# Performance work log

Measured on AMD Instinct MI355X. Metric: run time of the kernel, lower is better.

Reference implementation:

```python
import jax, jax.numpy as jnp
import numpy as np

N = 50000      # nodes
E = 800000     # edges (before self-loops)
F_IN = 256     # num_features
H = 8          # heads (conv1)
C = 32         # hidden_size per head (conv1)
OUT = 2        # conv2 out channels (1 head)
NEG_SLOPE = 0.2


def setup_inputs() -> dict:
    key = jax.random.key(0)
    ks = jax.random.split(key, 12)
    x = jax.random.normal(ks[0], (N, F_IN), jnp.float32)
    edge_index = jax.random.randint(ks[1], (2, E), 0, N, dtype=jnp.int64)

    def glorot(k, shape):
        fan = shape[0] if len(shape) == 2 else int(np.prod(shape))
        s = float(np.sqrt(6.0 / (fan + shape[-1])))
        return jax.random.uniform(k, shape, jnp.float32, -s, s)

    W1 = glorot(ks[2], (F_IN, H * C))
    att_src1 = glorot(ks[3], (H, C))
    att_dst1 = glorot(ks[4], (H, C))
    b1 = jnp.zeros((H * C,), jnp.float32)
    W2 = glorot(ks[5], (H * C, 1 * OUT))
    att_src2 = glorot(ks[6], (1, OUT))
    att_dst2 = glorot(ks[7], (1, OUT))
    b2 = jnp.zeros((OUT,), jnp.float32)
    return {"x": x, "edge_index": edge_index, "W1": W1, "att_src1": att_src1,
            "att_dst1": att_dst1, "b1": b1, "W2": W2, "att_src2": att_src2,
            "att_dst2": att_dst2, "b2": b2}


def gat_conv(x, src, dst, W, a_src, a_dst, b, heads, ch, n):
    # x: [n, f] -> projected [n, heads, ch]
    xp = (x @ W).reshape(n, heads, ch)
    alpha_src = jnp.einsum('nhc,hc->nh', xp, a_src)   # [n, H]
    alpha_dst = jnp.einsum('nhc,hc->nh', xp, a_dst)   # [n, H]
    e = jax.nn.leaky_relu(alpha_src[src] + alpha_dst[dst], NEG_SLOPE)  # [E', H]
    # segment softmax over edges grouped by destination node
    m = jax.ops.segment_max(e, dst, num_segments=n)                    # [n, H]
    p = jnp.exp(e - m[dst])
    denom = jax.ops.segment_sum(p, dst, num_segments=n)                # [n, H]
    alpha = p / denom[dst]                                             # [E', H]
    # weighted scatter-aggregate of source messages
    out = jax.ops.segment_sum(xp[src] * alpha[:, :, None], dst, num_segments=n)
    return out.reshape(n, heads * ch) + b


def reference(x, edge_index, W1, att_src1, att_dst1, b1, W2, att_src2, att_dst2, b2):
    n = x.shape[0]
    loops = jnp.arange(n, dtype=edge_index.dtype)  # GATConv add_self_loops=True
    src = jnp.concatenate([edge_index[0], loops])
    dst = jnp.concatenate([edge_index[1], loops])
    h = jax.nn.relu(gat_conv(x, src, dst, W1, att_src1, att_dst1, b1, H, C, n))
    # eval mode: F.dropout and attention dropout are identity
    return gat_conv(h, src, dst, W2, att_src2, att_dst2, b2, 1, OUT, n)
```

## Files before the change

kernel.cpp:

```cpp
#include <hip/hip_runtime.h>
#include <math.h>

#define N_NODES 50000
#define N_EDGES 800000
#define EP (N_EDGES + N_NODES)
#define NEG 0.2f
#define SCAN_BLOCKS 49

typedef __attribute__((ext_vector_type(8))) short bf16x8;
typedef __attribute__((ext_vector_type(4))) float f32x4;
typedef __attribute__((ext_vector_type(2))) float f32x2;

static __device__ __forceinline__ unsigned short bf16_rn(float f) {
    union { float f; unsigned int u; } v; v.f = f;
    unsigned int u = v.u;
    unsigned int r = (u + 0x7FFFu + ((u >> 16) & 1u)) >> 16;
    return (unsigned short)r;
}
static __device__ __forceinline__ float bf16_tof(unsigned short u) {
    union { unsigned int u; float f; } v; v.u = ((unsigned int)u) << 16;
    return v.f;
}
static __device__ __forceinline__ f32x2 bf2_unpack(unsigned int u) {
    union { unsigned int i; float f; } a, b;
    a.i = u << 16; b.i = u & 0xFFFF0000u;
    return (f32x2){a.f, b.f};
}


__global__ void k_hist(const int* __restrict__ ei, int* __restrict__ counts) {
    int e = blockIdx.x * 256 + threadIdx.x;
    if (e >= EP) return;
    int d = (e < N_EDGES) ? ei[N_EDGES + e] : (e - N_EDGES);
    atomicAdd(&counts[d], 1);
}

__global__ void k_scan_block(const int* __restrict__ counts, int* __restrict__ excl,
                             int* __restrict__ bsums) {
    __shared__ int wsum[4];
    int b = blockIdx.x, t = threadIdx.x;
    int lane = t & 63, w = t >> 6;
    int i0 = b * 1024 + t * 4;
    int v0 = (i0 + 0 < N_NODES) ? counts[i0 + 0] : 0;
    int v1 = (i0 + 1 < N_NODES) ? counts[i0 + 1] : 0;
    int v2 = (i0 + 2 < N_NODES) ? counts[i0 + 2] : 0;
    int v3 = (i0 + 3 < N_NODES) ? counts[i0 + 3] : 0;
    int s = v0 + v1 + v2 + v3;
    int incl = s;
    #pragma unroll
    for (int d = 1; d < 64; d <<= 1) {
        int u = __shfl_up(incl, d);
        if (lane >= d) incl += u;
    }
    if (lane == 63) wsum[w] = incl;
    __syncthreads();
    if (t == 0) {
        int run = 0;
        #pragma unroll
        for (int i = 0; i < 4; ++i) { int x = wsum[i]; wsum[i] = run; run += x; }
        bsums[b] = run;
    }
    __syncthreads();
    int base = wsum[w] + incl - s;
    if (i0 + 0 < N_NODES) excl[i0 + 0] = base;
    if (i0 + 1 < N_NODES) excl[i0 + 1] = base + v0;
    if (i0 + 2 < N_NODES) excl[i0 + 2] = base + v0 + v1;
    if (i0 + 3 < N_NODES) excl[i0 + 3] = base + v0 + v1 + v2;
}

__global__ void k_scan_add(int* __restrict__ row_ptr, const int* __restrict__ bsums) {
    __shared__ int soff;
    int b = blockIdx.x, t = threadIdx.x;
    if (t < 64) {
        int v = (t < SCAN_BLOCKS) ? bsums[t] : 0;
        int incl = v;
        #pragma unroll
        for (int d = 1; d < 64; d <<= 1) {
            int u = __shfl_up(incl, d);
            if (t >= d) incl += u;
        }
        if (t == b) soff = incl - v;
    }
    __syncthreads();
    int off = soff;
    int i0 = b * 1024 + t * 4;
    #pragma unroll
    for (int j = 0; j < 4; ++j)
        if (i0 + j < N_NODES) row_ptr[i0 + j] += off;
    if (b == 0 && t == 0) row_ptr[N_NODES] = EP;
}

__global__ void k_scatter(const int* __restrict__ ei, const int* __restrict__ row_ptr,
                          int* __restrict__ fill, int* __restrict__ colb) {
    int e = blockIdx.x * 256 + threadIdx.x;
    if (e >= EP) return;
    int s, d;
    if (e < N_EDGES) { s = ei[e]; d = ei[N_EDGES + e]; }
    else             { s = e - N_EDGES; d = s; }
    int pos = row_ptr[d] + atomicAdd(&fill[d], 1);
    colb[pos] = s;
}

__global__ void k_cvtWfrag(const float* __restrict__ W1, bf16x8* __restrict__ Wfrag) {
    int ft = blockIdx.x * 256 + threadIdx.x;
    int c = ft >> 10, rem = ft & 1023;
    int nt = rem >> 6, l = rem & 63;
    int n = (l & 15) * 16 + nt;
    int k0 = c * 32 + (l >> 4) * 8;
    bf16x8 f;
    #pragma unroll
    for (int j = 0; j < 8; ++j)
        f[j] = (short)bf16_rn(W1[(k0 + j) * 256 + n]);
    Wfrag[ft] = f;
}

#define GM_GRID 782
__global__ __launch_bounds__(128) void
k_gemm1m(const float* __restrict__ x, const bf16x8* __restrict__ Wfrag,
         unsigned short* __restrict__ xp1b,
         const float* __restrict__ asrc, const float* __restrict__ adst,
         float* __restrict__ as1, float* __restrict__ ad1) {
    __shared__ bf16x8 lds[1024];
    int t = threadIdx.x, l = t & 63, w = t >> 6;
    int rowbase = blockIdx.x * 64 + w * 32;
    int m = l & 15, kg = l >> 4;

    f32x4 acc0[16], acc1[16];
    #pragma unroll
    for (int nt = 0; nt < 16; ++nt) {
        acc0[nt] = (f32x4){0.f, 0.f, 0.f, 0.f};
        acc1[nt] = (f32x4){0.f, 0.f, 0.f, 0.f};
    }

    int r0 = rowbase + m;
    int r1 = rowbase + 16 + m;
    if (r0 > N_NODES - 1) r0 = N_NODES - 1;
    if (r1 > N_NODES - 1) r1 = N_NODES - 1;
    const float4* x4 = (const float4*)x;

    for (int c = 0; c < 8; ++c) {
        __syncthreads();
        const bf16x8* src = Wfrag + c * 1024;
        #pragma unroll
        for (int q = 0; q < 8; ++q)
            lds[q * 128 + t] = src[q * 128 + t];
        __syncthreads();

        int kb = (c * 32 + kg * 8) >> 2;
        float4 xa0 = x4[r0 * 64 + kb], xb0 = x4[r0 * 64 + kb + 1];
        float4 xa1 = x4[r1 * 64 + kb], xb1 = x4[r1 * 64 + kb + 1];
        bf16x8 aF0, aF1;
        aF0[0] = (short)bf16_rn(xa0.x); aF0[1] = (short)bf16_rn(xa0.y);
        aF0[2] = (short)bf16_rn(xa0.z); aF0[3] = (short)bf16_rn(xa0.w);
        aF0[4] = (short)bf16_rn(xb0.x); aF0[5] = (short)bf16_rn(xb0.y);
        aF0[6] = (short)bf16_rn(xb0.z); aF0[7] = (short)bf16_rn(xb0.w);
        aF1[0] = (short)bf16_rn(xa1.x); aF1[1] = (short)bf16_rn(xa1.y);
        aF1[2] = (short)bf16_rn(xa1.z); aF1[3] = (short)bf16_rn(xa1.w);
        aF1[4] = (short)bf16_rn(xb1.x); aF1[5] = (short)bf16_rn(xb1.y);
        aF1[6] = (short)bf16_rn(xb1.z); aF1[7] = (short)bf16_rn(xb1.w);

        #pragma unroll
        for (int nt = 0; nt < 16; ++nt) {
            bf16x8 bF = lds[nt * 64 + l];
            acc0[nt] = __builtin_amdgcn_mfma_f32_16x16x32_bf16(aF0, bF, acc0[nt], 0, 0, 0);
            acc1[nt] = __builtin_amdgcn_mfma_f32_16x16x32_bf16(aF1, bF, acc1[nt], 0, 0, 0);
        }
    }

    int cbase = l & 15, rq = l >> 4;
    float asV[16], adV[16];
    #pragma unroll
    for (int q = 0; q < 4; ++q) {
        float4 sa = ((const float4*)asrc)[cbase * 4 + q];
        float4 da = ((const float4*)adst)[cbase * 4 + q];
        asV[q * 4 + 0] = sa.x; asV[q * 4 + 1] = sa.y; asV[q * 4 + 2] = sa.z; asV[q * 4 + 3] = sa.w;
        adV[q * 4 + 0] = da.x; adV[q * 4 + 1] = da.y; adV[q * 4 + 2] = da.z; adV[q * 4 + 3] = da.w;
    }
    #pragma unroll
    for (int g = 0; g < 2; ++g) {
        f32x4* A = g ? acc1 : acc0;
        #pragma unroll
        for (int reg = 0; reg < 4; ++reg) {
            int gr = rowbase + g * 16 + rq * 4 + reg;
            unsigned int ob[8];
            float ps = 0.f, pd = 0.f;
            #pragma unroll
            for (int q = 0; q < 8; ++q) {
                float v0 = A[2 * q][reg], v1 = A[2 * q + 1][reg];
                ob[q] = (unsigned int)bf16_rn(v0) | ((unsigned int)bf16_rn(v1) << 16);
                ps = fmaf(v0, asV[2 * q], ps);     ps = fmaf(v1, asV[2 * q + 1], ps);
                pd = fmaf(v0, adV[2 * q], pd);     pd = fmaf(v1, adV[2 * q + 1], pd);
            }
            ps += __shfl_xor(ps, 1);
            pd += __shfl_xor(pd, 1);
            if (gr < N_NODES) {
                uint4* dst = (uint4*)(xp1b + gr * 256 + cbase * 16);
                dst[0] = make_uint4(ob[0], ob[1], ob[2], ob[3]);
                dst[1] = make_uint4(ob[4], ob[5], ob[6], ob[7]);
                if ((l & 1) == 0) {
                    as1[gr * 8 + (cbase >> 1)] = ps;
                    ad1[gr * 8 + (cbase >> 1)] = pd;
                }
            }
        }
    }
}

__global__ void k_agg1(const ushort4* __restrict__ xpb, const float* __restrict__ as1,
                       const float* __restrict__ ad1, const int* __restrict__ row_ptr,
                       const int* __restrict__ colb, const float* __restrict__ b1,
                       const float* __restrict__ W2, const float* __restrict__ as2w,
                       const float* __restrict__ ad2w,
                       float* __restrict__ xp2, float* __restrict__ as2,
                       float* __restrict__ ad2) {
    int t = threadIdx.x, l = t & 63, w = t >> 6;
    int n = blockIdx.x * 4 + w;
    int hidx = l >> 3;
    float adn = ad1[n * 8 + hidx];
    int start = row_ptr[n], end = row_ptr[n + 1];
    const uint2* xp2v = (const uint2*)xpb;
    f32x2 accA = {0.f, 0.f}, accB = {0.f, 0.f};
    float den = 0.f;
    int j = start;
    for (; j + 4 <= end; j += 4) {
        int s0 = colb[j], s1 = colb[j + 1], s2 = colb[j + 2], s3 = colb[j + 3];
        uint2 r0 = xp2v[s0 * 64 + l];
        uint2 r1 = xp2v[s1 * 64 + l];
        uint2 r2 = xp2v[s2 * 64 + l];
        uint2 r3 = xp2v[s3 * 64 + l];
        float e0 = as1[s0 * 8 + hidx] + adn;
        float e1 = as1[s1 * 8 + hidx] + adn;
        float e2 = as1[s2 * 8 + hidx] + adn;
        float e3 = as1[s3 * 8 + hidx] + adn;
        e0 = (e0 > 0.f) ? e0 : NEG * e0;
        e1 = (e1 > 0.f) ? e1 : NEG * e1;
        e2 = (e2 > 0.f) ? e2 : NEG * e2;
        e3 = (e3 > 0.f) ? e3 : NEG * e3;
        float p0 = __expf(e0), p1 = __expf(e1), p2 = __expf(e2), p3 = __expf(e3);
        den += (p0 + p1) + (p2 + p3);
        f32x2 q0 = {p0, p0}, q1 = {p1, p1}, q2 = {p2, p2}, q3 = {p3, p3};
        accA += q0 * bf2_unpack(r0.x);  accB += q0 * bf2_unpack(r0.y);
        accA += q1 * bf2_unpack(r1.x);  accB += q1 * bf2_unpack(r1.y);
        accA += q2 * bf2_unpack(r2.x);  accB += q2 * bf2_unpack(r2.y);
        accA += q3 * bf2_unpack(r3.x);  accB += q3 * bf2_unpack(r3.y);
    }
    for (; j < end; ++j) {
        int s = colb[j];
        uint2 r = xp2v[s * 64 + l];
        float e = as1[s * 8 + hidx] + adn;
        e = (e > 0.f) ? e : NEG * e;
        float p = __expf(e);
        den += p;
        f32x2 q = {p, p};
        accA += q * bf2_unpack(r.x);
        accB += q * bf2_unpack(r.y);
    }
    float4 bv = ((const float4*)b1)[l];
    float inv = 1.f / den;
    float4 o;
    o.x = fmaxf(accA[0] * inv + bv.x, 0.f);
    o.y = fmaxf(accA[1] * inv + bv.y, 0.f);
    o.z = fmaxf(accB[0] * inv + bv.z, 0.f);
    o.w = fmaxf(accB[1] * inv + bv.w, 0.f);
    float4 wa = ((const float4*)W2)[2 * l];
    float4 wb = ((const float4*)W2)[2 * l + 1];
    float d0 = o.x * wa.x + o.y * wa.z + o.z * wb.x + o.w * wb.z;
    float d1 = o.x * wa.y + o.y * wa.w + o.z * wb.y + o.w * wb.w;
    #pragma unroll
    for (int m = 1; m < 64; m <<= 1) {
        d0 += __shfl_xor(d0, m);
        d1 += __shfl_xor(d1, m);
    }
    if (l == 0) {
        xp2[2 * n] = d0;
        xp2[2 * n + 1] = d1;
        as2[n] = d0 * as2w[0] + d1 * as2w[1];
        ad2[n] = d0 * ad2w[0] + d1 * ad2w[1];
    }
}

__global__ void k_agg2(const float* __restrict__ xp2, const float* __restrict__ as2,
                       const float* __restrict__ ad2, const int* __restrict__ row_ptr,
                       const int* __restrict__ colb, const float* __restrict__ b2,
                       float* __restrict__ out) {
    int t = threadIdx.x, l = t & 63, w = t >> 6;
    int n = blockIdx.x * 4 + w;
    int start = row_ptr[n], end = row_ptr[n + 1];
    float adn = ad2[n];
    float a0 = 0.f, a1 = 0.f, den = 0.f;
    for (int j = start + l; j < end; j += 64) {
        int s = colb[j];
        float e = as2[s] + adn;
        e = (e > 0.f) ? e : NEG * e;
        float p = __expf(e);
        den += p;
        a0 = fmaf(p, xp2[2 * s], a0);
        a1 = fmaf(p, xp2[2 * s + 1], a1);
    }
    #pragma unroll
    for (int m = 1; m < 64; m <<= 1) {
        a0 += __shfl_xor(a0, m);
        a1 += __shfl_xor(a1, m);
        den += __shfl_xor(den, m);
    }
    if (l == 0) {
        out[2 * n] = a0 / den + b2[0];
        out[2 * n + 1] = a1 / den + b2[1];
    }
}

extern "C" void kernel_launch(void* const* d_in, const int* in_sizes, int n_in,
                              void* d_out, int out_size, void* d_ws, size_t ws_size,
                              hipStream_t stream) {
    const float* x     = (const float*)d_in[0];
    const int*   ei    = (const int*)d_in[1];
    const float* W1    = (const float*)d_in[2];
    const float* asrc1 = (const float*)d_in[3];
    const float* adst1 = (const float*)d_in[4];
    const float* b1    = (const float*)d_in[5];
    const float* W2    = (const float*)d_in[6];
    const float* asrc2 = (const float*)d_in[7];
    const float* adst2 = (const float*)d_in[8];
    const float* b2    = (const float*)d_in[9];
    float* out = (float*)d_out;

    char* ws = (char*)d_ws;
    unsigned short* xp1b = (unsigned short*)(ws + 0);
    bf16x8* Wfrag  = (bf16x8*)(ws + 25600000);
    float* as1     = (float*)(ws + 102400000);
    float* ad1     = (float*)(ws + 104000000);
    float* xp2     = (float*)(ws + 105600000);
    float* as2     = (float*)(ws + 106000000);
    float* ad2     = (float*)(ws + 106200000);
    int*   counts  = (int*)  (ws + 106400000);
    int*   fill    = (int*)  (ws + 106600000);
    int*   row_ptr = (int*)  (ws + 106800000);
    int*   colb    = (int*)  (ws + 107000064);
    int*   bsums   = (int*)  (ws + 110400064);

    hipMemsetAsync(counts, 0, 400000, stream);

    int egrid = (EP + 255) / 256;
    k_hist      <<<egrid,       256, 0, stream>>>(ei, counts);
    k_scan_block<<<SCAN_BLOCKS, 256, 0, stream>>>(counts, row_ptr, bsums);
    k_scan_add  <<<SCAN_BLOCKS, 256, 0, stream>>>(row_ptr, bsums);
    k_scatter   <<<egrid,       256, 0, stream>>>(ei, row_ptr, fill, colb);

    k_cvtWfrag  <<<32,     256, 0, stream>>>(W1, Wfrag);
    k_gemm1m    <<<GM_GRID, 128, 0, stream>>>(x, Wfrag, xp1b, asrc1, adst1, as1, ad1);
    k_agg1      <<<12500,  256, 0, stream>>>((const ushort4*)xp1b, as1, ad1, row_ptr, colb,
                                             b1, W2, asrc2, adst2, xp2, as2, ad2);
    k_agg2      <<<12500,  256, 0, stream>>>(xp2, as2, ad2, row_ptr, colb, b2, out);
}
```

Measured before the change: 294.1 us.

## Rebalance thread mapping in GEMM and both aggregation kernels

The GEMM now uses 256 threads per block, with each wave computing 16 rows instead of 32. This halves the accumulator registers per thread and splits the LDS fill across more threads. In agg1, each half-wave handles alternate edges with 16-byte feature loads, and the two halves are combined with a cross-half shuffle. agg2 uses 16 lanes per node instead of 64, packing 16 nodes per block, and loads each xp2 pair as one float2. The aim is better occupancy and memory-level parallelism, at the cost of extra shuffle reductions and, in agg1, padded lanes on nodes with odd edge counts.

```diff
diff --git a/kernel.cpp b/kernel.cpp
--- a/kernel.cpp
+++ b/kernel.cpp
@@ -115,55 +115,45 @@
 }
 
 #define GM_GRID 782
-__global__ __launch_bounds__(128) void
+__global__ __launch_bounds__(256) void
 k_gemm1m(const float* __restrict__ x, const bf16x8* __restrict__ Wfrag,
          unsigned short* __restrict__ xp1b,
          const float* __restrict__ asrc, const float* __restrict__ adst,
          float* __restrict__ as1, float* __restrict__ ad1) {
     __shared__ bf16x8 lds[1024];
     int t = threadIdx.x, l = t & 63, w = t >> 6;
-    int rowbase = blockIdx.x * 64 + w * 32;
+    int rowbase = blockIdx.x * 64 + w * 16;
     int m = l & 15, kg = l >> 4;
 
-    f32x4 acc0[16], acc1[16];
-    #pragma unroll
-    for (int nt = 0; nt < 16; ++nt) {
-        acc0[nt] = (f32x4){0.f, 0.f, 0.f, 0.f};
-        acc1[nt] = (f32x4){0.f, 0.f, 0.f, 0.f};
-    }
+    f32x4 acc[16];
+    #pragma unroll
+    for (int nt = 0; nt < 16; ++nt)
+        acc[nt] = (f32x4){0.f, 0.f, 0.f, 0.f};
 
     int r0 = rowbase + m;
-    int r1 = rowbase + 16 + m;
     if (r0 > N_NODES - 1) r0 = N_NODES - 1;
-    if (r1 > N_NODES - 1) r1 = N_NODES - 1;
     const float4* x4 = (const float4*)x;
 
     for (int c = 0; c < 8; ++c) {
         __syncthreads();
         const bf16x8* src = Wfrag + c * 1024;
         #pragma unroll
-        for (int q = 0; q < 8; ++q)
-            lds[q * 128 + t] = src[q * 128 + t];
+        for (int q = 0; q < 4; ++q)
+            lds[q * 256 + t] = src[q * 256 + t];
         __syncthreads();
 
         int kb = (c * 32 + kg * 8) >> 2;
         float4 xa0 = x4[r0 * 64 + kb], xb0 = x4[r0 * 64 + kb + 1];
-        float4 xa1 = x4[r1 * 64 + kb], xb1 = x4[r1 * 64 + kb + 1];
-        bf16x8 aF0, aF1;
+        bf16x8 aF0;
         aF0[0] = (short)bf16_rn(xa0.x); aF0[1] = (short)bf16_rn(xa0.y);
         aF0[2] = (short)bf16_rn(xa0.z); aF0[3] = (short)bf16_rn(xa0.w);
         aF0[4] = (short)bf16_rn(xb0.x); aF0[5] = (short)bf16_rn(xb0.y);
         aF0[6] = (short)bf16_rn(xb0.z); aF0[7] = (short)bf16_rn(xb0.w);
-        aF1[0] = (short)bf16_rn(xa1.x); aF1[1] = (short)bf16_rn(xa1.y);
-        aF1[2] = (short)bf16_rn(xa1.z); aF1[3] = (short)bf16_rn(xa1.w);
-        aF1[4] = (short)bf16_rn(xb1.x); aF1[5] = (short)bf16_rn(xb1.y);
-        aF1[6] = (short)bf16_rn(xb1.z); aF1[7] = (short)bf16_rn(xb1.w);
 
         #pragma unroll
         for (int nt = 0; nt < 16; ++nt) {
             bf16x8 bF = lds[nt * 64 + l];
-            acc0[nt] = __builtin_amdgcn_mfma_f32_16x16x32_bf16(aF0, bF, acc0[nt], 0, 0, 0);
-            acc1[nt] = __builtin_amdgcn_mfma_f32_16x16x32_bf16(aF1, bF, acc1[nt], 0, 0, 0);
+            acc[nt] = __builtin_amdgcn_mfma_f32_16x16x32_bf16(aF0, bF, acc[nt], 0, 0, 0);
         }
     }
 
@@ -177,30 +167,26 @@
         adV[q * 4 + 0] = da.x; adV[q * 4 + 1] = da.y; adV[q * 4 + 2] = da.z; adV[q * 4 + 3] = da.w;
     }
     #pragma unroll
-    for (int g = 0; g < 2; ++g) {
-        f32x4* A = g ? acc1 : acc0;
-        #pragma unroll
-        for (int reg = 0; reg < 4; ++reg) {
-            int gr = rowbase + g * 16 + rq * 4 + reg;
-            unsigned int ob[8];
-            float ps = 0.f, pd = 0.f;
-            #pragma unroll
-            for (int q = 0; q < 8; ++q) {
-                float v0 = A[2 * q][reg], v1 = A[2 * q + 1][reg];
-                ob[q] = (unsigned int)bf16_rn(v0) | ((unsigned int)bf16_rn(v1) << 16);
-                ps = fmaf(v0, asV[2 * q], ps);     ps = fmaf(v1, asV[2 * q + 1], ps);
-                pd = fmaf(v0, adV[2 * q], pd);     pd = fmaf(v1, adV[2 * q + 1], pd);
-            }
-            ps += __shfl_xor(ps, 1);
-            pd += __shfl_xor(pd, 1);
-            if (gr < N_NODES) {
-                uint4* dst = (uint4*)(xp1b + gr * 256 + cbase * 16);
-                dst[0] = make_uint4(ob[0], ob[1], ob[2], ob[3]);
-                dst[1] = make_uint4(ob[4], ob[5], ob[6], ob[7]);
-                if ((l & 1) == 0) {
-                    as1[gr * 8 + (cbase >> 1)] = ps;
-                    ad1[gr * 8 + (cbase >> 1)] = pd;
-                }
+    for (int reg = 0; reg < 4; ++reg) {
+        int gr = rowbase + rq * 4 + reg;
+        unsigned int ob[8];
+        float ps = 0.f, pd = 0.f;
+        #pragma unroll
+        for (int q = 0; q < 8; ++q) {
+            float v0 = acc[2 * q][reg], v1 = acc[2 * q + 1][reg];
+            ob[q] = (unsigned int)bf16_rn(v0) | ((unsigned int)bf16_rn(v1) << 16);
+            ps = fmaf(v0, asV[2 * q], ps);     ps = fmaf(v1, asV[2 * q + 1], ps);
+            pd = fmaf(v0, adV[2 * q], pd);     pd = fmaf(v1, adV[2 * q + 1], pd);
+        }
+        ps += __shfl_xor(ps, 1);
+        pd += __shfl_xor(pd, 1);
+        if (gr < N_NODES) {
+            uint4* dst = (uint4*)(xp1b + gr * 256 + cbase * 16);
+            dst[0] = make_uint4(ob[0], ob[1], ob[2], ob[3]);
+            dst[1] = make_uint4(ob[4], ob[5], ob[6], ob[7]);
+            if ((l & 1) == 0) {
+                as1[gr * 8 + (cbase >> 1)] = ps;
+                ad1[gr * 8 + (cbase >> 1)] = pd;
             }
         }
     }
@@ -215,59 +201,73 @@
                        float* __restrict__ ad2) {
     int t = threadIdx.x, l = t & 63, w = t >> 6;
     int n = blockIdx.x * 4 + w;
-    int hidx = l >> 3;
+    int hl = l & 31;
+    int half = l >> 5;
+    int hidx = hl >> 2;
     float adn = ad1[n * 8 + hidx];
     int start = row_ptr[n], end = row_ptr[n + 1];
-    const uint2* xp2v = (const uint2*)xpb;
-    f32x2 accA = {0.f, 0.f}, accB = {0.f, 0.f};
+    const uint4* xp4 = (const uint4*)xpb;
+    f32x2 acc0 = {0.f, 0.f}, acc1 = {0.f, 0.f}, acc2 = {0.f, 0.f}, acc3 = {0.f, 0.f};
     float den = 0.f;
     int j = start;
     for (; j + 4 <= end; j += 4) {
-        int s0 = colb[j], s1 = colb[j + 1], s2 = colb[j + 2], s3 = colb[j + 3];
-        uint2 r0 = xp2v[s0 * 64 + l];
-        uint2 r1 = xp2v[s1 * 64 + l];
-        uint2 r2 = xp2v[s2 * 64 + l];
-        uint2 r3 = xp2v[s3 * 64 + l];
+        int jj0 = j + half, jj1 = j + 2 + half;
+        int s0 = colb[jj0], s1 = colb[jj1];
+        uint4 r0 = xp4[s0 * 32 + hl];
+        uint4 r1 = xp4[s1 * 32 + hl];
         float e0 = as1[s0 * 8 + hidx] + adn;
         float e1 = as1[s1 * 8 + hidx] + adn;
-        float e2 = as1[s2 * 8 + hidx] + adn;
-        float e3 = as1[s3 * 8 + hidx] + adn;
         e0 = (e0 > 0.f) ? e0 : NEG * e0;
         e1 = (e1 > 0.f) ? e1 : NEG * e1;
-        e2 = (e2 > 0.f) ? e2 : NEG * e2;
-        e3 = (e3 > 0.f) ? e3 : NEG * e3;
-        float p0 = __expf(e0), p1 = __expf(e1), p2 = __expf(e2), p3 = __expf(e3);
-        den += (p0 + p1) + (p2 + p3);
-        f32x2 q0 = {p0, p0}, q1 = {p1, p1}, q2 = {p2, p2}, q3 = {p3, p3};
-        accA += q0 * bf2_unpack(r0.x);  accB += q0 * bf2_unpack(r0.y);
-        accA += q1 * bf2_unpack(r1.x);  accB += q1 * bf2_unpack(r1.y);
-        accA += q2 * bf2_unpack(r2.x);  accB += q2 * bf2_unpack(r2.y);
-        accA += q3 * bf2_unpack(r3.x);  accB += q3 * bf2_unpack(r3.y);
-    }
-    for (; j < end; ++j) {
-        int s = colb[j];
-        uint2 r = xp2v[s * 64 + l];
+        float p0 = __expf(e0), p1 = __expf(e1);
+        den += p0 + p1;
+        f32x2 q0 = {p0, p0}, q1 = {p1, p1};
+        acc0 += q0 * bf2_unpack(r0.x);  acc1 += q0 * bf2_unpack(r0.y);
+        acc2 += q0 * bf2_unpack(r0.z);  acc3 += q0 * bf2_unpack(r0.w);
+        acc0 += q1 * bf2_unpack(r1.x);  acc1 += q1 * bf2_unpack(r1.y);
+        acc2 += q1 * bf2_unpack(r1.z);  acc3 += q1 * bf2_unpack(r1.w);
+    }
+    for (; j < end; j += 2) {
+        int jj = j + half;
+        bool v = jj < end;
+        int s = colb[v ? jj : start];
+        uint4 r = xp4[s * 32 + hl];
         float e = as1[s * 8 + hidx] + adn;
         e = (e > 0.f) ? e : NEG * e;
-        float p = __expf(e);
+        float p = v ? __expf(e) : 0.f;
         den += p;
         f32x2 q = {p, p};
-        accA += q * bf2_unpack(r.x);
-        accB += q * bf2_unpack(r.y);
-    }
-    float4 bv = ((const float4*)b1)[l];
+        acc0 += q * bf2_unpack(r.x);  acc1 += q * bf2_unpack(r.y);
+        acc2 += q * bf2_unpack(r.z);  acc3 += q * bf2_unpack(r.w);
+    }
+    acc0[0] += __shfl_xor(acc0[0], 32); acc0[1] += __shfl_xor(acc0[1], 32);
+    acc1[0] += __shfl_xor(acc1[0], 32); acc1[1] += __shfl_xor(acc1[1], 32);
+    acc2[0] += __shfl_xor(acc2[0], 32); acc2[1] += __shfl_xor(acc2[1], 32);
+    acc3[0] += __shfl_xor(acc3[0], 32); acc3[1] += __shfl_xor(acc3[1], 32);
+    den += __shfl_xor(den, 32);
+
     float inv = 1.f / den;
-    float4 o;
-    o.x = fmaxf(accA[0] * inv + bv.x, 0.f);
-    o.y = fmaxf(accA[1] * inv + bv.y, 0.f);
-    o.z = fmaxf(accB[0] * inv + bv.z, 0.f);
-    o.w = fmaxf(accB[1] * inv + bv.w, 0.f);
-    float4 wa = ((const float4*)W2)[2 * l];
-    float4 wb = ((const float4*)W2)[2 * l + 1];
-    float d0 = o.x * wa.x + o.y * wa.z + o.z * wb.x + o.w * wb.z;
-    float d1 = o.x * wa.y + o.y * wa.w + o.z * wb.y + o.w * wb.w;
-    #pragma unroll
-    for (int m = 1; m < 64; m <<= 1) {
+    float4 ba = ((const float4*)b1)[hl * 2];
+    float4 bb = ((const float4*)b1)[hl * 2 + 1];
+    float o0 = fmaxf(acc0[0] * inv + ba.x, 0.f);
+    float o1 = fmaxf(acc0[1] * inv + ba.y, 0.f);
+    float o2 = fmaxf(acc1[0] * inv + ba.z, 0.f);
+    float o3 = fmaxf(acc1[1] * inv + ba.w, 0.f);
+    float o4 = fmaxf(acc2[0] * inv + bb.x, 0.f);
+    float o5 = fmaxf(acc2[1] * inv + bb.y, 0.f);
+    float o6 = fmaxf(acc3[0] * inv + bb.z, 0.f);
+    float o7 = fmaxf(acc3[1] * inv + bb.w, 0.f);
+    const float4* W4 = (const float4*)W2;
+    float4 wa = W4[hl * 4 + 0];
+    float4 wb = W4[hl * 4 + 1];
+    float4 wc = W4[hl * 4 + 2];
+    float4 wd = W4[hl * 4 + 3];
+    float d0 = o0 * wa.x + o1 * wa.z + o2 * wb.x + o3 * wb.z
+             + o4 * wc.x + o5 * wc.z + o6 * wd.x + o7 * wd.z;
+    float d1 = o0 * wa.y + o1 * wa.w + o2 * wb.y + o3 * wb.w
+             + o4 * wc.y + o5 * wc.w + o6 * wd.y + o7 * wd.w;
+    #pragma unroll
+    for (int m = 1; m < 32; m <<= 1) {
         d0 += __shfl_xor(d0, m);
         d1 += __shfl_xor(d1, m);
     }
@@ -283,27 +283,29 @@
                        const float* __restrict__ ad2, const int* __restrict__ row_ptr,
                        const int* __restrict__ colb, const float* __restrict__ b2,
                        float* __restrict__ out) {
-    int t = threadIdx.x, l = t & 63, w = t >> 6;
-    int n = blockIdx.x * 4 + w;
+    int t = threadIdx.x;
+    int g = t >> 4, lane = t & 15;
+    int n = blockIdx.x * 16 + g;
     int start = row_ptr[n], end = row_ptr[n + 1];
     float adn = ad2[n];
     float a0 = 0.f, a1 = 0.f, den = 0.f;
-    for (int j = start + l; j < end; j += 64) {
+    for (int j = start + lane; j < end; j += 16) {
         int s = colb[j];
         float e = as2[s] + adn;
         e = (e > 0.f) ? e : NEG * e;
         float p = __expf(e);
         den += p;
-        a0 = fmaf(p, xp2[2 * s], a0);
-        a1 = fmaf(p, xp2[2 * s + 1], a1);
-    }
-    #pragma unroll
-    for (int m = 1; m < 64; m <<= 1) {
+        float2 xv = ((const float2*)xp2)[s];
+        a0 = fmaf(p, xv.x, a0);
+        a1 = fmaf(p, xv.y, a1);
+    }
+    #pragma unroll
+    for (int m = 1; m < 16; m <<= 1) {
         a0 += __shfl_xor(a0, m);
         a1 += __shfl_xor(a1, m);
         den += __shfl_xor(den, m);
     }
-    if (l == 0) {
+    if (lane == 0) {
         out[2 * n] = a0 / den + b2[0];
         out[2 * n + 1] = a1 / den + b2[1];
     }
@@ -347,8 +349,8 @@
     k_scatter   <<<egrid,       256, 0, stream>>>(ei, row_ptr, fill, colb);
 
     k_cvtWfrag  <<<32,     256, 0, stream>>>(W1, Wfrag);
-    k_gemm1m    <<<GM_GRID, 128, 0, stream>>>(x, Wfrag, xp1b, asrc1, adst1, as1, ad1);
+    k_gemm1m    <<<GM_GRID, 256, 0, stream>>>(x, Wfrag, xp1b, asrc1, adst1, as1, ad1);
     k_agg1      <<<12500,  256, 0, stream>>>((const ushort4*)xp1b, as1, ad1, row_ptr, colb,
                                              b1, W2, asrc2, adst2, xp2, as2, ad2);
-    k_agg2      <<<12500,  256, 0, stream>>>(xp2, as2, ad2, row_ptr, colb, b2, out);
-}
+    k_agg2      <<<3125,   256, 0, stream>>>(xp2, as2, ad2, row_ptr, colb, b2, out);
+}
```

Measured after the change: 294.1 us. About the same (-0.0%).
